# Kernel tuning notes

Hardware: AMD Instinct MI355X
Metric: run time of the kernel (lower is better)

## Reference

```python
import jax, jax.numpy as jnp
import numpy as np

N = 100000       # nodes
E = 1200000      # edges (before self loops)
IN = 3
H = 64           # hidden
HNUM = 256       # number of direct virtual nodes
L = 2            # layers - 1 (hidden GATConvs and VN MLPs)
NEG_SLOPE = 0.2  # GATConv default


def setup_inputs() -> dict:
    key = jax.random.key(0)
    ks = jax.random.split(key, 20)
    s_in = 1.0 / np.sqrt(IN)
    s_h = 1.0 / np.sqrt(H)
    inp = dict(
        x=jax.random.normal(ks[0], (N, IN), dtype=jnp.float32),
        edge_index=jax.random.randint(ks[1], (2, E), 0, N, dtype=jnp.int32),
        h_blocks=jax.random.randint(ks[2], (N,), 0, HNUM, dtype=jnp.int32),
        h_levels=jax.random.randint(ks[3], (N,), 0, 4, dtype=jnp.int32),
        h_num=HNUM,
        # initial GATConv(IN -> H)
        w_in=jax.random.normal(ks[4], (IN, H), dtype=jnp.float32) * s_in,
        a_src_in=jax.random.normal(ks[5], (H,), dtype=jnp.float32) * s_h,
        a_dst_in=jax.random.normal(ks[6], (H,), dtype=jnp.float32) * s_h,
        b_in=jnp.zeros((H,), dtype=jnp.float32),
        # L hidden GATConv(H -> H) layers, stacked
        w_l=jax.random.normal(ks[7], (L, H, H), dtype=jnp.float32) * s_h,
        a_src_l=jax.random.normal(ks[8], (L, H), dtype=jnp.float32) * s_h,
        a_dst_l=jax.random.normal(ks[9], (L, H), dtype=jnp.float32) * s_h,
        b_l=jnp.zeros((L, H), dtype=jnp.float32),
        # L virtual-node MLPs: Linear-ReLU-Linear-ReLU
        mlp_w1=jax.random.normal(ks[10], (L, H, H), dtype=jnp.float32) * s_h,
        mlp_b1=jnp.zeros((L, H), dtype=jnp.float32),
        mlp_w2=jax.random.normal(ks[11], (L, H, H), dtype=jnp.float32) * s_h,
        mlp_b2=jnp.zeros((L, H), dtype=jnp.float32),
        # virtualnode embedding, constant-initialized to 0 in original
        vn_emb=jnp.zeros((1, H), dtype=jnp.float32),
    )
    return inp


def _gat_conv(x, src, dst, n, W, a_src, a_dst, b):
    """PyG GATConv, heads=1, add_self_loops already in (src,dst)."""
    h = x @ W                                   # [n, H]
    alpha = jax.nn.leaky_relu((h @ a_src)[src] + (h @ a_dst)[dst], NEG_SLOPE)
    # softmax over incoming edges of each dst node (self-loops => nonempty)
    amax = jax.ops.segment_max(alpha, dst, num_segments=n)
    ex = jnp.exp(alpha - amax[dst])
    denom = jax.ops.segment_sum(ex, dst, num_segments=n)
    w = ex / denom[dst]                         # [E_total]
    out = jax.ops.segment_sum(w[:, None] * h[src], dst, num_segments=n)
    return out + b


def _mlp(v, w1, b1, w2, b2):
    return jax.nn.relu(jax.nn.relu(v @ w1 + b1) @ w2 + b2)


def reference(x, edge_index, h_blocks, h_levels, h_num,
              w_in, a_src_in, a_dst_in, b_in,
              w_l, a_src_l, a_dst_l, b_l,
              mlp_w1, mlp_b1, mlp_w2, mlp_b2, vn_emb):
    n = x.shape[0]
    loops = jnp.arange(n, dtype=edge_index.dtype)
    src = jnp.concatenate([edge_index[0], loops])
    dst = jnp.concatenate([edge_index[1], loops])

    out = _gat_conv(x, src, dst, n, w_in, a_src_in, a_dst_in, b_in)
    vn_direct = jnp.broadcast_to(vn_emb, (h_num, vn_emb.shape[1]))  # zeros init
    vn_root = vn_emb                                                # [1, H]

    for l in range(L):
        out = out + vn_direct[h_blocks]
        out = _gat_conv(out, src, dst, n, w_l[l], a_src_l[l], a_dst_l[l], b_l[l])
        vn_direct = jax.ops.segment_sum(out, h_blocks, num_segments=h_num) + vn_direct
        vn_direct = vn_direct + vn_root
        vn_root = jnp.sum(vn_direct, axis=0, keepdims=True) + vn_root
        # original applies ALL vn MLPs each layer (faithful reproduction)
        for m in range(L):
            vn_direct = _mlp(vn_direct, mlp_w1[m], mlp_b1[m], mlp_w2[m], mlp_b2[m])
            vn_root = _mlp(vn_root, mlp_w1[m], mlp_b1[m], mlp_w2[m], mlp_b2[m])
    return out
```

## Files before the change

### kernel.cpp

```cpp
#include <hip/hip_runtime.h>


typedef __attribute__((ext_vector_type(8))) short short8;
typedef __attribute__((ext_vector_type(4))) float f32x4;

__device__ __forceinline__ unsigned short f2bf(float x){
    unsigned u = __float_as_uint(x);
    unsigned r = (u + 0x7fffu + ((u >> 16) & 1u)) >> 16;
    return (unsigned short)r;
}
__device__ __forceinline__ float bf2f(unsigned short b){
    return __uint_as_float(((unsigned)b) << 16);
}

#define BSHIFT 9
#define CHUNK 4096
#define NSLICE 8

__device__ __forceinline__ int incl_scan256(int v, int* sums4){
    int lane = threadIdx.x & 63, w = threadIdx.x >> 6;
    int x = v;
    #pragma unroll
    for (int o = 1; o < 64; o <<= 1){ int t = __shfl_up(x, o, 64); if (lane >= o) x += t; }
    __syncthreads();
    if (lane == 63) sums4[w] = x;
    __syncthreads();
    for (int j = 0; j < w; ++j) x += sums4[j];
    return x;
}

__global__ __launch_bounds__(256) void k_count(const int* __restrict__ dst, int E, int NB,
                                               int* __restrict__ bucketCount,
                                               const int* __restrict__ hb, int N,
                                               int* __restrict__ hbBins){
    __shared__ int cnt[256], cnt2[256];
    cnt[threadIdx.x] = 0; cnt2[threadIdx.x] = 0;
    __syncthreads();
    int base = blockIdx.x*CHUNK;
    int lim = min(base + CHUNK, E);
    for (int i = base + threadIdx.x; i < lim; i += 256)
        atomicAdd(&cnt[dst[i] >> BSHIFT], 1);
    int limN = min(base + CHUNK, N);
    for (int i = base + threadIdx.x; i < limN; i += 256)
        atomicAdd(&cnt2[hb[i]], 1);
    __syncthreads();
    if (threadIdx.x < NB && cnt[threadIdx.x])
        atomicAdd(&bucketCount[threadIdx.x], cnt[threadIdx.x]);
    if (cnt2[threadIdx.x])
        atomicAdd(&hbBins[threadIdx.x], cnt2[threadIdx.x]);
}

__global__ __launch_bounds__(256) void k_scan_all(const int* __restrict__ bucketCount,
                                                  int NB, int E, int N,
                                                  int* __restrict__ bucketOff,
                                                  int* __restrict__ bucketCur,
                                                  int* __restrict__ rowptr,
                                                  const int* __restrict__ hbBins,
                                                  int* __restrict__ binptr,
                                                  int* __restrict__ bincur){
    __shared__ int sums4[4];
    int tid = threadIdx.x;
    int v = (tid < NB) ? bucketCount[tid] : 0;
    int x = incl_scan256(v, sums4);
    if (tid < NB){ bucketOff[tid] = x - v; bucketCur[tid] = x - v; }
    if (tid == NB-1) bucketOff[NB] = x;
    if (tid == 0) rowptr[N] = E;
    int v2 = hbBins[tid];
    int x2 = incl_scan256(v2, sums4);
    binptr[tid] = x2 - v2;
    bincur[tid] = x2 - v2;
    if (tid == 255) binptr[256] = x2;
}

__global__ __launch_bounds__(256) void k_bucket_place(const int* __restrict__ src,
                                                      const int* __restrict__ dst, int E, int NB,
                                                      int* __restrict__ bucketCur,
                                                      int2* __restrict__ pairs){
    __shared__ int cnt[256], binStart[256], binCur[256], chunkBase[256];
    __shared__ int sums4[4];
    __shared__ int2 lp[CHUNK];
    int tid = threadIdx.x;
    cnt[tid] = 0; binCur[tid] = 0;
    __syncthreads();
    int base = blockIdx.x*CHUNK;
    int s[16], d[16];
    #pragma unroll
    for (int k = 0; k < 16; ++k){
        int i = base + k*256 + tid;
        if (i < E){ s[k] = src[i]; d[k] = dst[i]; atomicAdd(&cnt[d[k] >> BSHIFT], 1); }
        else d[k] = -1;
    }
    __syncthreads();
    int v = cnt[tid];
    int x = incl_scan256(v, sums4);
    binStart[tid] = x - v;
    __syncthreads();
    #pragma unroll
    for (int k = 0; k < 16; ++k){
        if (d[k] >= 0){
            int b = d[k] >> BSHIFT;
            int p = binStart[b] + atomicAdd(&binCur[b], 1);
            lp[p] = make_int2(s[k], d[k]);
        }
    }
    if (tid < NB){
        int c = cnt[tid];
        chunkBase[tid] = c ? atomicAdd(&bucketCur[tid], c) : 0;
    }
    __syncthreads();
    int total = min(CHUNK, E - base);
    for (int i = tid; i < total; i += 256){
        int2 p = lp[i];
        int b = p.y >> BSHIFT;
        pairs[chunkBase[b] + (i - binStart[b])] = p;
    }
}

__global__ __launch_bounds__(256) void k_hb_place(const int* __restrict__ hb, int N,
                                                  int* __restrict__ bincur,
                                                  int* __restrict__ nodes){
    __shared__ int cnt[256], binStart[256], binCur[256], chunkBase[256];
    __shared__ int sums4[4];
    __shared__ int lp[CHUNK];
    __shared__ unsigned char lb[CHUNK];
    int tid = threadIdx.x;
    cnt[tid] = 0; binCur[tid] = 0;
    __syncthreads();
    int base = blockIdx.x*CHUNK;
    int key[16];
    #pragma unroll
    for (int k = 0; k < 16; ++k){
        int i = base + k*256 + tid;
        key[k] = (i < N) ? hb[i] : -1;
        if (key[k] >= 0) atomicAdd(&cnt[key[k]], 1);
    }
    __syncthreads();
    int v = cnt[tid];
    int x = incl_scan256(v, sums4);
    binStart[tid] = x - v;
    __syncthreads();
    #pragma unroll
    for (int k = 0; k < 16; ++k){
        if (key[k] >= 0){
            int p = binStart[key[k]] + atomicAdd(&binCur[key[k]], 1);
            lp[p] = base + k*256 + tid;
            lb[p] = (unsigned char)key[k];
        }
    }
    if (cnt[tid]) chunkBase[tid] = atomicAdd(&bincur[tid], cnt[tid]);
    __syncthreads();
    int total = min(CHUNK, N - base);
    for (int i = tid; i < total; i += 256){
        int b = lb[i];
        nodes[chunkBase[b] + (i - binStart[b])] = lp[i];
    }
}

__global__ __launch_bounds__(256) void k_bucket_csr(const int2* __restrict__ pairs,
                                                    const int* __restrict__ bucketOff, int N,
                                                    int* __restrict__ rowptr,
                                                    int* __restrict__ colarr){
    __shared__ int deg[512], cur[512];
    __shared__ int sums4[4];
    __shared__ int tAs;
    int b = blockIdx.x, tid = threadIdx.x;
    int d0 = b << BSHIFT;
    int e0 = bucketOff[b], e1 = bucketOff[b+1];
    deg[tid] = 0; deg[256+tid] = 0;
    __syncthreads();
    for (int i = e0 + tid; i < e1; i += 256)
        atomicAdd(&deg[pairs[i].y - d0], 1);
    __syncthreads();
    int vA = deg[tid], vB = deg[256+tid];
    int xA = incl_scan256(vA, sums4);
    if (tid == 255) tAs = xA;
    int xB = incl_scan256(vB, sums4) + tAs;
    int exclA = xA - vA, exclB = xB - vB;
    cur[tid] = exclA; cur[256+tid] = exclB;
    int dA = d0 + tid, dB = d0 + 256 + tid;
    if (dA < N) rowptr[dA] = e0 + exclA;
    if (dB < N) rowptr[dB] = e0 + exclB;
    __syncthreads();
    for (int i = e0 + tid; i < e1; i += 256){
        int2 p = pairs[i];
        int pos = e0 + atomicAdd(&cur[p.y - d0], 1);
        colarr[pos] = p.x;
    }
}

__global__ __launch_bounds__(256) void k_transform_in(const float* __restrict__ x,
                                                      const float* __restrict__ W,
                                                      const float* __restrict__ a_src,
                                                      const float* __restrict__ a_dst,
                                                      unsigned short* __restrict__ hout,
                                                      float* __restrict__ ssrc,
                                                      float* __restrict__ sdst, int N){
    int wv = blockIdx.x*4 + (threadIdx.x >> 6);
    int lane = threadIdx.x & 63;
    if (wv >= N) return;
    float acc = 0.f;
    #pragma unroll
    for (int k = 0; k < 3; ++k)
        acc += x[wv*3 + k] * W[k*64 + lane];
    hout[(size_t)wv*64 + lane] = f2bf(acc);
    float v1 = acc * a_src[lane];
    float v2 = acc * a_dst[lane];
    #pragma unroll
    for (int o = 32; o; o >>= 1){ v1 += __shfl_xor(v1, o, 64); v2 += __shfl_xor(v2, o, 64); }
    if (lane == 0){ ssrc[wv] = v1; sdst[wv] = v2; }
}

#define LDW 72
__global__ __launch_bounds__(256) void k_transform_h_mfma(const float* __restrict__ feat,
                                                          const float* __restrict__ vn,
                                                          const float* __restrict__ vn_emb,
                                                          const int* __restrict__ hb,
                                                          const float* __restrict__ W,
                                                          const float* __restrict__ a_src,
                                                          const float* __restrict__ a_dst,
                                                          unsigned short* __restrict__ hout,
                                                          float* __restrict__ ssrc,
                                                          float* __restrict__ sdst, int N){
    __shared__ unsigned short WhT[64*LDW], WlT[64*LDW], Ah[64*LDW], Al[64*LDW];
    const int n0 = blockIdx.x * 64;

    for (int idx = threadIdx.x; idx < 4096; idx += 256){
        int n = idx >> 6, k = idx & 63;
        float w = W[k*64 + n];
        unsigned short hi = f2bf(w);
        WhT[n*LDW + k] = hi;
        WlT[n*LDW + k] = f2bf(w - bf2f(hi));
    }
    for (int t = threadIdx.x; t < 1024; t += 256){
        int row = t >> 4, c4 = t & 15;
        int node = n0 + row;
        float4 v = make_float4(0.f,0.f,0.f,0.f);
        if (node < N){
            v = ((const float4*)feat)[(size_t)node*16 + c4];
            float4 g = vn ? ((const float4*)vn)[(size_t)hb[node]*16 + c4]
                          : ((const float4*)vn_emb)[c4];
            v.x += g.x; v.y += g.y; v.z += g.z; v.w += g.w;
        }
        int base = row*LDW + c4*4;
        unsigned short h0 = f2bf(v.x), h1 = f2bf(v.y), h2 = f2bf(v.z), h3 = f2bf(v.w);
        Ah[base+0] = h0; Al[base+0] = f2bf(v.x - bf2f(h0));
        Ah[base+1] = h1; Al[base+1] = f2bf(v.y - bf2f(h1));
        Ah[base+2] = h2; Al[base+2] = f2bf(v.z - bf2f(h2));
        Ah[base+3] = h3; Al[base+3] = f2bf(v.w - bf2f(h3));
    }
    __syncthreads();

    int lane = threadIdx.x & 63;
    int wv   = threadIdx.x >> 6;
    int mrow = lane & 15, quad = lane >> 4;
    int m0 = wv * 16;

    f32x4 acc0 = {0,0,0,0}, acc1 = {0,0,0,0}, acc2 = {0,0,0,0}, acc3 = {0,0,0,0};
    #pragma unroll
    for (int k0 = 0; k0 < 64; k0 += 32){
        int kb = k0 + quad*8;
        short8 ah = *(const short8*)&Ah[(m0+mrow)*LDW + kb];
        short8 al = *(const short8*)&Al[(m0+mrow)*LDW + kb];
        short8 b0h = *(const short8*)&WhT[( 0+mrow)*LDW + kb];
        short8 b1h = *(const short8*)&WhT[(16+mrow)*LDW + kb];
        short8 b2h = *(const short8*)&WhT[(32+mrow)*LDW + kb];
        short8 b3h = *(const short8*)&WhT[(48+mrow)*LDW + kb];
        short8 b0l = *(const short8*)&WlT[( 0+mrow)*LDW + kb];
        short8 b1l = *(const short8*)&WlT[(16+mrow)*LDW + kb];
        short8 b2l = *(const short8*)&WlT[(32+mrow)*LDW + kb];
        short8 b3l = *(const short8*)&WlT[(48+mrow)*LDW + kb];
        acc0 = __builtin_amdgcn_mfma_f32_16x16x32_bf16(ah, b0h, acc0, 0, 0, 0);
        acc1 = __builtin_amdgcn_mfma_f32_16x16x32_bf16(ah, b1h, acc1, 0, 0, 0);
        acc2 = __builtin_amdgcn_mfma_f32_16x16x32_bf16(ah, b2h, acc2, 0, 0, 0);
        acc3 = __builtin_amdgcn_mfma_f32_16x16x32_bf16(ah, b3h, acc3, 0, 0, 0);
        acc0 = __builtin_amdgcn_mfma_f32_16x16x32_bf16(ah, b0l, acc0, 0, 0, 0);
        acc1 = __builtin_amdgcn_mfma_f32_16x16x32_bf16(ah, b1l, acc1, 0, 0, 0);
        acc2 = __builtin_amdgcn_mfma_f32_16x16x32_bf16(ah, b2l, acc2, 0, 0, 0);
        acc3 = __builtin_amdgcn_mfma_f32_16x16x32_bf16(ah, b3l, acc3, 0, 0, 0);
        acc0 = __builtin_amdgcn_mfma_f32_16x16x32_bf16(al, b0h, acc0, 0, 0, 0);
        acc1 = __builtin_amdgcn_mfma_f32_16x16x32_bf16(al, b1h, acc1, 0, 0, 0);
        acc2 = __builtin_amdgcn_mfma_f32_16x16x32_bf16(al, b2h, acc2, 0, 0, 0);
        acc3 = __builtin_amdgcn_mfma_f32_16x16x32_bf16(al, b3h, acc3, 0, 0, 0);
    }

    float as0 = a_src[mrow], as1 = a_src[16+mrow], as2 = a_src[32+mrow], as3 = a_src[48+mrow];
    float ad0 = a_dst[mrow], ad1 = a_dst[16+mrow], ad2 = a_dst[32+mrow], ad3 = a_dst[48+mrow];
    #pragma unroll
    for (int r = 0; r < 4; ++r){
        float p1 = acc0[r]*as0 + acc1[r]*as1 + acc2[r]*as2 + acc3[r]*as3;
        float p2 = acc0[r]*ad0 + acc1[r]*ad1 + acc2[r]*ad2 + acc3[r]*ad3;
        #pragma unroll
        for (int o = 8; o; o >>= 1){ p1 += __shfl_xor(p1, o, 64); p2 += __shfl_xor(p2, o, 64); }
        int node = n0 + m0 + quad*4 + r;
        if (mrow == 0 && node < N){ ssrc[node] = p1; sdst[node] = p2; }
    }
    #pragma unroll
    for (int r = 0; r < 4; ++r){
        int row = m0 + quad*4 + r;
        Ah[row*LDW + mrow     ] = f2bf(acc0[r]);
        Ah[row*LDW + mrow + 16] = f2bf(acc1[r]);
        Ah[row*LDW + mrow + 32] = f2bf(acc2[r]);
        Ah[row*LDW + mrow + 48] = f2bf(acc3[r]);
    }
    int r2 = lane >> 2, seg = lane & 3;
    int node = n0 + m0 + r2;
    if (node < N){
        short8 va = *(const short8*)&Ah[(m0+r2)*LDW + seg*16];
        short8 vb = *(const short8*)&Ah[(m0+r2)*LDW + seg*16 + 8];
        *(short8*)&hout[(size_t)node*64 + seg*16]     = va;
        *(short8*)&hout[(size_t)node*64 + seg*16 + 8] = vb;
    }
}

__global__ __launch_bounds__(256) void k_aggregate(const unsigned short* __restrict__ h,
                                                   const float* __restrict__ ssrc,
                                                   const float* __restrict__ sdst,
                                                   const int* __restrict__ rowptr,
                                                   const int* __restrict__ col,
                                                   const float* __restrict__ bias,
                                                   float* __restrict__ out, int N){
    __shared__ float2 swb[4][64];
    int wv = threadIdx.x >> 6;
    int lane = threadIdx.x & 63;
    int half = lane >> 5, lane32 = lane & 31;
    int d = blockIdx.x*8 + wv*2 + half;
    if (d >= N) return;
    int r8 = lane32 >> 3, c8 = lane32 & 7;
    float sd = sdst[d];
    float a0 = ssrc[d] + sd; a0 = (a0 < 0.f) ? 0.2f*a0 : a0;
    float dlocal = 0.f;
    float acc[8] = {0,0,0,0,0,0,0,0};
    if (r8 == 0){
        uint4 u = *(const uint4*)&h[(size_t)d*64 + c8*8];
        acc[0] = __uint_as_float(u.x << 16); acc[1] = __uint_as_float(u.x & 0xffff0000u);
        acc[2] = __uint_as_float(u.y << 16); acc[3] = __uint_as_float(u.y & 0xffff0000u);
        acc[4] = __uint_as_float(u.z << 16); acc[5] = __uint_as_float(u.z & 0xffff0000u);
        acc[6] = __uint_as_float(u.w << 16); acc[7] = __uint_as_float(u.w & 0xffff0000u);
    }
    int e0 = rowptr[d], e1 = rowptr[d+1];
    for (int base = e0; base < e1; base += 32){
        int ne = min(32, e1 - base);
        float w = 0.f; int s = 0;
        if (lane32 < ne){
            s = col[base + lane32];
            float a = ssrc[s] + sd;
            a = (a < 0.f) ? 0.2f*a : a;
            w = __expf(a - a0);
        }
        dlocal += w;
        swb[wv][lane] = make_float2(w, __int_as_float(s));
        int nj = (ne + 3) >> 2;
        for (int j = 0; j < nj; j += 2){
            float2 p0 = swb[wv][half*32 + j*4 + r8];
            float2 p1 = swb[wv][half*32 + j*4 + 4 + r8];
            int s0 = __float_as_int(p0.y);
            int s1 = __float_as_int(p1.y);
            uint4 u0 = *(const uint4*)&h[(size_t)s0*64 + c8*8];
            uint4 u1 = *(const uint4*)&h[(size_t)s1*64 + c8*8];
            acc[0] += p0.x * __uint_as_float(u0.x << 16);
            acc[1] += p0.x * __uint_as_float(u0.x & 0xffff0000u);
            acc[2] += p0.x * __uint_as_float(u0.y << 16);
            acc[3] += p0.x * __uint_as_float(u0.y & 0xffff0000u);
            acc[4] += p0.x * __uint_as_float(u0.z << 16);
            acc[5] += p0.x * __uint_as_float(u0.z & 0xffff0000u);
            acc[6] += p0.x * __uint_as_float(u0.w << 16);
            acc[7] += p0.x * __uint_as_float(u0.w & 0xffff0000u);
            acc[0] += p1.x * __uint_as_float(u1.x << 16);
            acc[1] += p1.x * __uint_as_float(u1.x & 0xffff0000u);
            acc[2] += p1.x * __uint_as_float(u1.y << 16);
            acc[3] += p1.x * __uint_as_float(u1.y & 0xffff0000u);
            acc[4] += p1.x * __uint_as_float(u1.z << 16);
            acc[5] += p1.x * __uint_as_float(u1.z & 0xffff0000u);
            acc[6] += p1.x * __uint_as_float(u1.w << 16);
            acc[7] += p1.x * __uint_as_float(u1.w & 0xffff0000u);
        }
    }
    #pragma unroll
    for (int o = 16; o; o >>= 1) dlocal += __shfl_xor(dlocal, o, 64);
    float denom = 1.0f + dlocal;
    #pragma unroll
    for (int o = 8; o <= 16; o <<= 1){
        #pragma unroll
        for (int k = 0; k < 8; ++k) acc[k] += __shfl_xor(acc[k], o, 64);
    }
    if (r8 == 0){
        float inv = 1.0f/denom;
        float4 b4a = ((const float4*)bias)[c8*2];
        float4 b4b = ((const float4*)bias)[c8*2 + 1];
        float4 o1 = make_float4(acc[0]*inv + b4a.x, acc[1]*inv + b4a.y,
                                acc[2]*inv + b4a.z, acc[3]*inv + b4a.w);
        float4 o2 = make_float4(acc[4]*inv + b4b.x, acc[5]*inv + b4b.y,
                                acc[6]*inv + b4b.z, acc[7]*inv + b4b.w);
        ((float4*)out)[(size_t)d*16 + c8*2    ] = o1;
        ((float4*)out)[(size_t)d*16 + c8*2 + 1] = o2;
    }
}

__global__ __launch_bounds__(256) void k_vn_segsum2(const float* __restrict__ outA,
                                                    const int* __restrict__ nodes,
                                                    const int* __restrict__ binptr,
                                                    float* __restrict__ vseg){
    __shared__ float part[4][64];
    int b = blockIdx.x >> 3, s = blockIdx.x & (NSLICE-1);
    int wv = threadIdx.x >> 6, lane = threadIdx.x & 63;
    int i0 = binptr[b], i1 = binptr[b+1];
    int len = i1 - i0;
    int lo = i0 + (len*s)/NSLICE;
    int hi = i0 + (len*(s+1))/NSLICE;
    float acc = 0.f;
    for (int i = lo + wv; i < hi; i += 4){
        int n = nodes[i];
        acc += outA[(size_t)n*64 + lane];
    }
    part[wv][lane] = acc;
    __syncthreads();
    if (threadIdx.x < 64)
        vseg[(size_t)blockIdx.x*64 + lane] =
            part[0][lane] + part[1][lane] + part[2][lane] + part[3][lane];
}

__global__ __launch_bounds__(256) void k_vn_combine(const float* __restrict__ vseg,
                                                    const float* __restrict__ vd_old,
                                                    const float* __restrict__ root_old,
                                                    const float* __restrict__ vn_emb,
                                                    float* __restrict__ vw){
    __shared__ float part[4][64];
    int wv = threadIdx.x >> 6, lane = threadIdx.x & 63;
    float rold = root_old ? root_old[lane] : vn_emb[lane];
    float emb  = vn_emb[lane];
    float csum = 0.f;
    for (int b = wv*64; b < wv*64 + 64; ++b){
        float v = 0.f;
        #pragma unroll
        for (int s = 0; s < NSLICE; ++s)
            v += vseg[(size_t)(b*NSLICE + s)*64 + lane];
        v += (vd_old ? vd_old[b*64 + lane] : emb) + rold;
        vw[b*64 + lane] = v;
        csum += v;
    }
    part[wv][lane] = csum;
    __syncthreads();
    if (threadIdx.x < 64)
        vw[256*64 + lane] = part[0][lane] + part[1][lane] + part[2][lane] + part[3][lane] + rold;
}

__global__ __launch_bounds__(256) void k_vn_mlp(const float* __restrict__ mlp_w1,
                                                const float* __restrict__ mlp_b1,
                                                const float* __restrict__ mlp_w2,
                                                const float* __restrict__ mlp_b2,
                                                int L, float* __restrict__ vw){
    __shared__ float Wl[64*64];
    int wv = blockIdx.x*4 + (threadIdx.x >> 6);
    int lane = threadIdx.x & 63;
    bool valid = (wv < 257);
    float iv = valid ? vw[wv*64 + lane] : 0.f;
    for (int m = 0; m < L; ++m){
        #pragma unroll
        for (int half = 0; half < 2; ++half){
            const float* W    = (half ? mlp_w2 : mlp_w1) + (size_t)m*4096;
            const float* bias = (half ? mlp_b2 : mlp_b1) + (size_t)m*64;
            __syncthreads();
            for (int i = threadIdx.x; i < 4096; i += 256) Wl[i] = W[i];
            __syncthreads();
            float acc = bias[lane];
            #pragma unroll
            for (int k = 0; k < 64; ++k)
                acc += __shfl(iv, k, 64) * Wl[k*64 + lane];
            iv = fmaxf(acc, 0.f);
        }
    }
    if (valid) vw[wv*64 + lane] = iv;
}

extern "C" void kernel_launch(void* const* d_in, const int* in_sizes, int n_in,
                              void* d_out, int out_size, void* d_ws, size_t ws_size,
                              hipStream_t stream) {
    const int N = in_sizes[0] / 3;
    const int E = in_sizes[1] / 2;
    const int L = in_sizes[9] / (64*64);
    const int NB = (N + (1<<BSHIFT) - 1) >> BSHIFT;

    const float* x        = (const float*)d_in[0];
    const int*   edge     = (const int*)d_in[1];
    const int*   srcp     = edge;
    const int*   dstp     = edge + E;
    const int*   hb       = (const int*)d_in[2];
    const float* w_in     = (const float*)d_in[5];
    const float* a_src_in = (const float*)d_in[6];
    const float* a_dst_in = (const float*)d_in[7];
    const float* b_in     = (const float*)d_in[8];
    const float* w_l      = (const float*)d_in[9];
    const float* a_src_l  = (const float*)d_in[10];
    const float* a_dst_l  = (const float*)d_in[11];
    const float* b_l      = (const float*)d_in[12];
    const float* mlp_w1   = (const float*)d_in[13];
    const float* mlp_b1   = (const float*)d_in[14];
    const float* mlp_w2   = (const float*)d_in[15];
    const float* mlp_b2   = (const float*)d_in[16];
    const float* vn_emb   = (const float*)d_in[17];
    float*       out      = (float*)d_out;

    char* ws = (char*)d_ws;
    size_t off = 0;
    auto carve = [&](size_t bytes) -> char* {
        char* p = ws + off;
        off = (off + bytes + 255) & ~(size_t)255;
        return p;
    };
    unsigned short* h = (unsigned short*)carve((size_t)N*64*2);
    float* outA   = (float*)carve((size_t)N*64*4);
    float* ssrc   = (float*)carve((size_t)N*4);
    float* sdst   = (float*)carve((size_t)N*4);
    int*   rowptr = (int*)carve((size_t)(N+1)*4);
    char*  zstart = ws + off;
    int*   bucketCount = (int*)carve(256*4);
    int*   hbBins = (int*)carve(256*4);
    size_t zbytes = (size_t)((ws + off) - zstart);
    int*   bucketOff = (int*)carve(257*4);
    int*   bucketCur = (int*)carve(256*4);
    int*   binptr = (int*)carve(257*4);
    int*   bincur = (int*)carve(256*4);
    int*   colarr = (int*)carve((size_t)E*4);
    int*   nodes  = (int*)carve((size_t)N*4);
    float* vseg   = (float*)carve((size_t)256*NSLICE*64*4);
    float* vw     = (float*)carve((size_t)257*64*4);
    if (off > ws_size) return;
    int2* pairs = (int2*)h;

    hipMemsetAsync(zstart, 0, zbytes, stream);
    const int nchunkE = (E + CHUNK - 1) / CHUNK;
    const int nchunkN = (N + CHUNK - 1) / CHUNK;
    k_count       <<<nchunkE, 256, 0, stream>>>(dstp, E, NB, bucketCount, hb, N, hbBins);
    k_scan_all    <<<1, 256, 0, stream>>>(bucketCount, NB, E, N, bucketOff, bucketCur, rowptr,
                                          hbBins, binptr, bincur);
    k_bucket_place<<<nchunkE, 256, 0, stream>>>(srcp, dstp, E, NB, bucketCur, pairs);
    k_bucket_csr  <<<NB, 256, 0, stream>>>(pairs, bucketOff, N, rowptr, colarr);
    k_hb_place    <<<nchunkN, 256, 0, stream>>>(hb, N, bincur, nodes);

    const int nwb = (N + 3) / 4;
    const int nab = (N + 7) / 8;
    const int nmb = (N + 63) / 64;

    k_transform_in<<<nwb, 256, 0, stream>>>(x, w_in, a_src_in, a_dst_in, h, ssrc, sdst, N);
    k_aggregate<<<nab, 256, 0, stream>>>(h, ssrc, sdst, rowptr, colarr, b_in, outA, N);

    for (int l = 0; l < L; ++l){
        const float* vnp = (l == 0) ? nullptr : vw;
        k_transform_h_mfma<<<nmb, 256, 0, stream>>>(outA, vnp, vn_emb, hb,
                                                    w_l + (size_t)l*4096,
                                                    a_src_l + (size_t)l*64,
                                                    a_dst_l + (size_t)l*64,
                                                    h, ssrc, sdst, N);
        const bool last = (l == L-1);
        float* dst_buf = last ? out : outA;
        k_aggregate<<<nab, 256, 0, stream>>>(h, ssrc, sdst, rowptr, colarr,
                                             b_l + (size_t)l*64, dst_buf, N);
        if (!last){
            const float* vdo = (l == 0) ? nullptr : vw;
            const float* ro  = (l == 0) ? nullptr : (vw + 256*64);
            k_vn_segsum2<<<256*NSLICE, 256, 0, stream>>>(outA, nodes, binptr, vseg);
            k_vn_combine<<<1, 256, 0, stream>>>(vseg, vdo, ro, vn_emb, vw);
            k_vn_mlp<<<(257+3)/4, 256, 0, stream>>>(mlp_w1, mlp_b1, mlp_w2, mlp_b2, L, vw);
        }
    }
}
```

Baseline: 360.2 us.

## Assign 16 lanes per destination node in GAT aggregation with 4-way unrolled gathers

The aggregation kernel now maps 16 lanes to each destination node instead of 32, so a wavefront handles four nodes and a block handles sixteen. Edges are processed in chunks of 16, and the inner loop issues four independent row gathers per iteration instead of two. This targets lanes left idle on low-degree nodes (average about 13 incoming edges) and gives more memory-level parallelism per lane. The cross-lane reduction gets shorter, but each lane now accumulates more edges serially, and more padded work can occur when the edge count per pass is not a multiple of 8.

Result: faster. 352.4 us (-2.2%).

```diff
diff --git a/kernel.cpp b/kernel.cpp
--- a/kernel.cpp
+++ b/kernel.cpp
@@ -322,15 +322,15 @@
     __shared__ float2 swb[4][64];
     int wv = threadIdx.x >> 6;
     int lane = threadIdx.x & 63;
-    int half = lane >> 5, lane32 = lane & 31;
-    int d = blockIdx.x*8 + wv*2 + half;
+    int grp = lane >> 4, lane16 = lane & 15;
+    int d = blockIdx.x*16 + wv*4 + grp;
     if (d >= N) return;
-    int r8 = lane32 >> 3, c8 = lane32 & 7;
+    int r2 = lane16 >> 3, c8 = lane16 & 7;
     float sd = sdst[d];
     float a0 = ssrc[d] + sd; a0 = (a0 < 0.f) ? 0.2f*a0 : a0;
     float dlocal = 0.f;
     float acc[8] = {0,0,0,0,0,0,0,0};
-    if (r8 == 0){
+    if (r2 == 0){
         uint4 u = *(const uint4*)&h[(size_t)d*64 + c8*8];
         acc[0] = __uint_as_float(u.x << 16); acc[1] = __uint_as_float(u.x & 0xffff0000u);
         acc[2] = __uint_as_float(u.y << 16); acc[3] = __uint_as_float(u.y & 0xffff0000u);
@@ -338,25 +338,29 @@
         acc[6] = __uint_as_float(u.w << 16); acc[7] = __uint_as_float(u.w & 0xffff0000u);
     }
     int e0 = rowptr[d], e1 = rowptr[d+1];
-    for (int base = e0; base < e1; base += 32){
-        int ne = min(32, e1 - base);
+    for (int base = e0; base < e1; base += 16){
+        int ne = min(16, e1 - base);
         float w = 0.f; int s = 0;
-        if (lane32 < ne){
-            s = col[base + lane32];
+        if (lane16 < ne){
+            s = col[base + lane16];
             float a = ssrc[s] + sd;
             a = (a < 0.f) ? 0.2f*a : a;
             w = __expf(a - a0);
         }
         dlocal += w;
         swb[wv][lane] = make_float2(w, __int_as_float(s));
-        int nj = (ne + 3) >> 2;
-        for (int j = 0; j < nj; j += 2){
-            float2 p0 = swb[wv][half*32 + j*4 + r8];
-            float2 p1 = swb[wv][half*32 + j*4 + 4 + r8];
-            int s0 = __float_as_int(p0.y);
-            int s1 = __float_as_int(p1.y);
+        int nj = (ne + 1) >> 1;
+        for (int j = 0; j < nj; j += 4){
+            float2 p0 = swb[wv][grp*16 + (j+0)*2 + r2];
+            float2 p1 = swb[wv][grp*16 + (j+1)*2 + r2];
+            float2 p2 = swb[wv][grp*16 + (j+2)*2 + r2];
+            float2 p3 = swb[wv][grp*16 + (j+3)*2 + r2];
+            int s0 = __float_as_int(p0.y), s1 = __float_as_int(p1.y);
+            int s2 = __float_as_int(p2.y), s3 = __float_as_int(p3.y);
             uint4 u0 = *(const uint4*)&h[(size_t)s0*64 + c8*8];
             uint4 u1 = *(const uint4*)&h[(size_t)s1*64 + c8*8];
+            uint4 u2 = *(const uint4*)&h[(size_t)s2*64 + c8*8];
+            uint4 u3 = *(const uint4*)&h[(size_t)s3*64 + c8*8];
             acc[0] += p0.x * __uint_as_float(u0.x << 16);
             acc[1] += p0.x * __uint_as_float(u0.x & 0xffff0000u);
             acc[2] += p0.x * __uint_as_float(u0.y << 16);
@@ -373,17 +377,30 @@
             acc[5] += p1.x * __uint_as_float(u1.z & 0xffff0000u);
             acc[6] += p1.x * __uint_as_float(u1.w << 16);
             acc[7] += p1.x * __uint_as_float(u1.w & 0xffff0000u);
-        }
-    }
-    #pragma unroll
-    for (int o = 16; o; o >>= 1) dlocal += __shfl_xor(dlocal, o, 64);
+            acc[0] += p2.x * __uint_as_float(u2.x << 16);
+            acc[1] += p2.x * __uint_as_float(u2.x & 0xffff0000u);
+            acc[2] += p2.x * __uint_as_float(u2.y << 16);
+            acc[3] += p2.x * __uint_as_float(u2.y & 0xffff0000u);
+            acc[4] += p2.x * __uint_as_float(u2.z << 16);
+            acc[5] += p2.x * __uint_as_float(u2.z & 0xffff0000u);
+            acc[6] += p2.x * __uint_as_float(u2.w << 16);
+            acc[7] += p2.x * __uint_as_float(u2.w & 0xffff0000u);
+            acc[0] += p3.x * __uint_as_float(u3.x << 16);
+            acc[1] += p3.x * __uint_as_float(u3.x & 0xffff0000u);
+            acc[2] += p3.x * __uint_as_float(u3.y << 16);
+            acc[3] += p3.x * __uint_as_float(u3.y & 0xffff0000u);
+            acc[4] += p3.x * __uint_as_float(u3.z << 16);
+            acc[5] += p3.x * __uint_as_float(u3.z & 0xffff0000u);
+            acc[6] += p3.x * __uint_as_float(u3.w << 16);
+            acc[7] += p3.x * __uint_as_float(u3.w & 0xffff0000u);
+        }
+    }
+    #pragma unroll
+    for (int o = 8; o; o >>= 1) dlocal += __shfl_xor(dlocal, o, 64);
     float denom = 1.0f + dlocal;
     #pragma unroll
-    for (int o = 8; o <= 16; o <<= 1){
-        #pragma unroll
-        for (int k = 0; k < 8; ++k) acc[k] += __shfl_xor(acc[k], o, 64);
-    }
-    if (r8 == 0){
+    for (int k = 0; k < 8; ++k) acc[k] += __shfl_xor(acc[k], 8, 64);
+    if (r2 == 0){
         float inv = 1.0f/denom;
         float4 b4a = ((const float4*)bias)[c8*2];
         float4 b4b = ((const float4*)bias)[c8*2 + 1];
@@ -538,7 +555,7 @@
     k_hb_place    <<<nchunkN, 256, 0, stream>>>(hb, N, bincur, nodes);
 
     const int nwb = (N + 3) / 4;
-    const int nab = (N + 7) / 8;
+    const int nab = (N + 15) / 16;
     const int nmb = (N + 63) / 64;
 
     k_transform_in<<<nwb, 256, 0, stream>>>(x, w_in, a_src_in, a_dst_in, h, ssrc, sdst, N);
```
